# Kernel optimization log

Hardware: AMD Instinct MI355X
Metric: run time of the kernel (lower is better)

Reference implementation:

```python
import jax, jax.numpy as jnp
import numpy as np

N_NODES = 100000
NEG_SLOPE = 0.01  # F.leaky_relu default


def _gin_mean_layer(x, src, dst):
    """DGL GINConv(aggregator='mean', apply_func=None, eps=0, activation=leaky_relu).
    out = leaky_relu((1+eps)*x + mean_{in-neighbors} x_src), nodes with no in-edges get mean=0.
    """
    msg_sum = jax.ops.segment_sum(x[src], dst, num_segments=N_NODES)  # [N, D]
    deg = jax.ops.segment_sum(jnp.ones(src.shape, dtype=x.dtype), dst, num_segments=N_NODES)  # [N]
    mean = msg_sum / jnp.maximum(deg, 1.0)[:, None]
    return jax.nn.leaky_relu(x + mean, negative_slope=NEG_SLOPE)


def setup_inputs() -> dict:
    key = jax.random.key(0)
    k0, k1, k2, k3, k4 = jax.random.split(key, 5)
    n_edges = 640000
    d = 128
    return {
        "node_features": jax.random.normal(k0, (N_NODES, d), dtype=jnp.float32),
        "edges1_src": jax.random.randint(k1, (n_edges,), 0, N_NODES, dtype=jnp.int64),
        "edges1_dst": jax.random.randint(k2, (n_edges,), 0, N_NODES, dtype=jnp.int64),
        "edges2_src": jax.random.randint(k3, (n_edges,), 0, N_NODES, dtype=jnp.int64),
        "edges2_dst": jax.random.randint(k4, (n_edges,), 0, N_NODES, dtype=jnp.int64),
    }


def reference(node_features, edges1_src, edges1_dst, edges2_src, edges2_dst):
    h_AC1 = _gin_mean_layer(node_features, edges1_src, edges1_dst)
    h_CA1 = _gin_mean_layer(node_features, edges2_src, edges2_dst)
    h = jnp.concatenate((h_AC1, h_CA1), axis=1)  # [N, 2D]
    h_AC2 = _gin_mean_layer(h, edges1_src, edges1_dst)
    h_CA2 = _gin_mean_layer(h, edges2_src, edges2_dst)
    return jnp.concatenate((h_AC2, h_CA2), axis=1)  # [N, 4D]
```

## Files before the change

kernel.cpp:

```cpp
#include <hip/hip_runtime.h>

#define N_NODES 100000
#define NEG 0.01f
#define CAP 32

typedef float f4v __attribute__((ext_vector_type(4)));

__device__ __forceinline__ float lrelu(float v) { return v > 0.f ? v : NEG * v; }

__device__ __forceinline__ unsigned int f2bf(float f) {
    unsigned int x = __float_as_uint(f);
    return (x + 0x7fffu + ((x >> 16) & 1u)) >> 16;
}
__device__ __forceinline__ unsigned int pack2bf(float lo, float hi) {
    return f2bf(lo) | (f2bf(hi) << 16);
}
__device__ __forceinline__ float bf_lo(unsigned int u) { return __uint_as_float(u << 16); }
__device__ __forceinline__ float bf_hi(unsigned int u) { return __uint_as_float(u & 0xffff0000u); }

__device__ __forceinline__ void unpack8(uint4 u, float* f) {
    f[0] = bf_lo(u.x); f[1] = bf_hi(u.x);
    f[2] = bf_lo(u.y); f[3] = bf_hi(u.y);
    f[4] = bf_lo(u.z); f[5] = bf_hi(u.z);
    f[6] = bf_lo(u.w); f[7] = bf_hi(u.w);
}

__global__ void __launch_bounds__(256) build_and_convert(
        const int* __restrict__ s1, const int* __restrict__ d1a, int E1,
        const int* __restrict__ s2, const int* __restrict__ d2a, int E2,
        int* __restrict__ deg1, int* __restrict__ slots1,
        int* __restrict__ deg2, int* __restrict__ slots2,
        const float4* __restrict__ x, uint4* __restrict__ xb, int convBlocks) {
    int b = blockIdx.x;
    if (b < convBlocks) {
        int i = b * 256 + threadIdx.x;
        if (i >= N_NODES * 16) return;
        float4 v0 = x[2 * i];
        float4 v1 = x[2 * i + 1];
        uint4 p;
        p.x = pack2bf(v0.x, v0.y);
        p.y = pack2bf(v0.z, v0.w);
        p.z = pack2bf(v1.x, v1.y);
        p.w = pack2bf(v1.z, v1.w);
        xb[i] = p;
    } else {
        int i = (b - convBlocks) * 256 + threadIdx.x;
        if (i < E1) {
            int d = d1a[i];
            int pos = atomicAdd(&deg1[d], 1);
            if (pos < CAP) slots1[d * CAP + pos] = s1[i];
        }
        int k = i - E1;
        if (k >= 0 && k < E2) {
            int d = d2a[k];
            int pos = atomicAdd(&deg2[d], 1);
            if (pos < CAP) slots2[d * CAP + pos] = s2[k];
        }
    }
}

__global__ void __launch_bounds__(256) layer1(
        const uint4* __restrict__ x4,
        const int* __restrict__ deg1, const int* __restrict__ slots1,
        const int* __restrict__ deg2, const int* __restrict__ slots2,
        uint4* __restrict__ h4) {
    int gid = blockIdx.x * blockDim.x + threadIdx.x;
    int n = gid >> 6;
    if (n >= N_NODES) return;
    int lane = gid & 63;
    int t = lane & 15;
    int g = lane >> 4;

    uint4 xv = x4[(size_t)n * 16 + t];

    int d1 = deg1[n], d2 = deg2[n];
    int m1 = min(d1, CAP), m2 = min(d2, CAP);
    int M = m1 + m2;

    int idx = 0;
    if (lane < m1) idx = slots1[n * CAP + lane];
    else if (lane - m1 < m2) idx = slots2[n * CAP + (lane - m1)];

    float a[8] = {0.f, 0.f, 0.f, 0.f, 0.f, 0.f, 0.f, 0.f};
    float b[8] = {0.f, 0.f, 0.f, 0.f, 0.f, 0.f, 0.f, 0.f};

    int s0 = __shfl(idx, g);
    uint4 u = make_uint4(0u, 0u, 0u, 0u);
    if (g < M) u = x4[(size_t)s0 * 16 + t];
    for (int j0 = 0; j0 < M; j0 += 4) {
        uint4 cur = u;
        int jc = j0 + g;
        bool isA = jc < m1;
        int jn = jc + 4;
        int sn = __shfl(idx, jn & 63);
        u = make_uint4(0u, 0u, 0u, 0u);
        if (jn < M) u = x4[(size_t)sn * 16 + t];
        float f[8]; unpack8(cur, f);
        #pragma unroll
        for (int i = 0; i < 8; ++i) {
            a[i] += isA ? f[i] : 0.f;
            b[i] += isA ? 0.f : f[i];
        }
    }

    #pragma unroll
    for (int i = 0; i < 8; ++i) {
        a[i] += __shfl_xor(a[i], 16);
        a[i] += __shfl_xor(a[i], 32);
        b[i] += __shfl_xor(b[i], 16);
        b[i] += __shfl_xor(b[i], 32);
    }

    float xf[8]; unpack8(xv, xf);
    float r1 = 1.f / (float)max(d1, 1);
    float r2 = 1.f / (float)max(d2, 1);

    if (g == 0) {
        uint4 o;
        o.x = pack2bf(lrelu(xf[0] + a[0] * r1), lrelu(xf[1] + a[1] * r1));
        o.y = pack2bf(lrelu(xf[2] + a[2] * r1), lrelu(xf[3] + a[3] * r1));
        o.z = pack2bf(lrelu(xf[4] + a[4] * r1), lrelu(xf[5] + a[5] * r1));
        o.w = pack2bf(lrelu(xf[6] + a[6] * r1), lrelu(xf[7] + a[7] * r1));
        h4[(size_t)n * 32 + t] = o;
    } else if (g == 1) {
        uint4 o;
        o.x = pack2bf(lrelu(xf[0] + b[0] * r2), lrelu(xf[1] + b[1] * r2));
        o.y = pack2bf(lrelu(xf[2] + b[2] * r2), lrelu(xf[3] + b[3] * r2));
        o.z = pack2bf(lrelu(xf[4] + b[4] * r2), lrelu(xf[5] + b[5] * r2));
        o.w = pack2bf(lrelu(xf[6] + b[6] * r2), lrelu(xf[7] + b[7] * r2));
        h4[(size_t)n * 32 + 16 + t] = o;
    }
}

__global__ void __launch_bounds__(256) layer2(
        const uint4* __restrict__ h4,
        const int* __restrict__ deg1, const int* __restrict__ slots1,
        const int* __restrict__ deg2, const int* __restrict__ slots2,
        float4* __restrict__ out4) {
    int gid = blockIdx.x * blockDim.x + threadIdx.x;
    int n = gid >> 6;
    if (n >= N_NODES) return;
    int lane = gid & 63;
    int t = lane & 31;
    int g = lane >> 5;

    uint4 hv = h4[(size_t)n * 32 + t];

    int d1 = deg1[n], d2 = deg2[n];
    int m1 = min(d1, CAP), m2 = min(d2, CAP);
    int M = m1 + m2;

    int idx = 0;
    if (lane < m1) idx = slots1[n * CAP + lane];
    else if (lane - m1 < m2) idx = slots2[n * CAP + (lane - m1)];

    float a[8] = {0.f, 0.f, 0.f, 0.f, 0.f, 0.f, 0.f, 0.f};
    float b[8] = {0.f, 0.f, 0.f, 0.f, 0.f, 0.f, 0.f, 0.f};

    int s0 = __shfl(idx, g);
    uint4 u = make_uint4(0u, 0u, 0u, 0u);
    if (g < M) u = h4[(size_t)s0 * 32 + t];
    for (int j0 = 0; j0 < M; j0 += 2) {
        uint4 cur = u;
        int jc = j0 + g;
        bool isA = jc < m1;
        int jn = jc + 2;
        int sn = __shfl(idx, jn & 63);
        u = make_uint4(0u, 0u, 0u, 0u);
        if (jn < M) u = h4[(size_t)sn * 32 + t];
        float f[8]; unpack8(cur, f);
        #pragma unroll
        for (int i = 0; i < 8; ++i) {
            a[i] += isA ? f[i] : 0.f;
            b[i] += isA ? 0.f : f[i];
        }
    }

    #pragma unroll
    for (int i = 0; i < 8; ++i) {
        a[i] += __shfl_xor(a[i], 32);
        b[i] += __shfl_xor(b[i], 32);
    }

    float hf[8]; unpack8(hv, hf);
    float r1 = 1.f / (float)max(d1, 1);
    float r2 = 1.f / (float)max(d2, 1);

    f4v* ob = (f4v*)out4;
    if (g == 0) {
        f4v A0 = {lrelu(hf[0] + a[0] * r1), lrelu(hf[1] + a[1] * r1),
                  lrelu(hf[2] + a[2] * r1), lrelu(hf[3] + a[3] * r1)};
        f4v A1 = {lrelu(hf[4] + a[4] * r1), lrelu(hf[5] + a[5] * r1),
                  lrelu(hf[6] + a[6] * r1), lrelu(hf[7] + a[7] * r1)};
        __builtin_nontemporal_store(A0, &ob[(size_t)n * 128 + 2 * t]);
        __builtin_nontemporal_store(A1, &ob[(size_t)n * 128 + 2 * t + 1]);
    } else {
        f4v B0 = {lrelu(hf[0] + b[0] * r2), lrelu(hf[1] + b[1] * r2),
                  lrelu(hf[2] + b[2] * r2), lrelu(hf[3] + b[3] * r2)};
        f4v B1 = {lrelu(hf[4] + b[4] * r2), lrelu(hf[5] + b[5] * r2),
                  lrelu(hf[6] + b[6] * r2), lrelu(hf[7] + b[7] * r2)};
        __builtin_nontemporal_store(B0, &ob[(size_t)n * 128 + 64 + 2 * t]);
        __builtin_nontemporal_store(B1, &ob[(size_t)n * 128 + 64 + 2 * t + 1]);
    }
}

extern "C" void kernel_launch(void* const* d_in, const int* in_sizes, int n_in,
                              void* d_out, int out_size, void* d_ws, size_t ws_size,
                              hipStream_t stream) {
    const float* x = (const float*)d_in[0];
    const int* e1s = (const int*)d_in[1];
    const int* e1d = (const int*)d_in[2];
    const int* e2s = (const int*)d_in[3];
    const int* e2d = (const int*)d_in[4];
    const int E1 = in_sizes[1];
    const int E2 = in_sizes[3];
    float* out = (float*)d_out;

    int* deg1   = (int*)d_ws;
    int* deg2   = deg1 + N_NODES;
    int* slots1 = deg2 + N_NODES;
    int* slots2 = slots1 + (size_t)N_NODES * CAP;
    unsigned int* xb = (unsigned int*)(slots2 + (size_t)N_NODES * CAP);
    unsigned int* hb = xb + (size_t)N_NODES * 64;

    hipMemsetAsync(deg1, 0, 2ull * N_NODES * sizeof(int), stream);

    int convBlocks = (N_NODES * 16 + 255) / 256;
    int edgeBlocks = (E1 + E2 + 255) / 256;
    build_and_convert<<<convBlocks + edgeBlocks, 256, 0, stream>>>(
        e1s, e1d, E1, e2s, e2d, E2, deg1, slots1, deg2, slots2,
        (const float4*)x, (uint4*)xb, convBlocks);

    int blocks = (N_NODES + 3) / 4;
    layer1<<<blocks, 256, 0, stream>>>(
        (const uint4*)xb, deg1, slots1, deg2, slots2, (uint4*)hb);
    layer2<<<blocks, 256, 0, stream>>>(
        (const uint4*)hb, deg1, slots1, deg2, slots2, (float4*)out);
}
```

Before: 521.7 us.

## Batch edge inserts per thread, deepen gather prefetch, load slot lists unconditionally

The edge-building phase now processes several edges per thread with an unrolled loop, and its blocks are scheduled before the bf16 conversion blocks so the atomic-heavy work starts first. Both layer kernels load the two slot lists unconditionally and merge them with a shuffle, which removes the dependent branchy loads. The neighbor-gather loop now keeps two loads in flight instead of one, to hide more of the random-gather latency. The costs are higher register pressure and reads of unused slot entries.

```diff
diff --git a/kernel.cpp b/kernel.cpp
--- a/kernel.cpp
+++ b/kernel.cpp
@@ -3,6 +3,7 @@
 #define N_NODES 100000
 #define NEG 0.01f
 #define CAP 32
+#define EDGE_ILP 8
 
 typedef float f4v __attribute__((ext_vector_type(4)));
 
@@ -30,10 +31,28 @@
         const int* __restrict__ s2, const int* __restrict__ d2a, int E2,
         int* __restrict__ deg1, int* __restrict__ slots1,
         int* __restrict__ deg2, int* __restrict__ slots2,
-        const float4* __restrict__ x, uint4* __restrict__ xb, int convBlocks) {
+        const float4* __restrict__ x, uint4* __restrict__ xb,
+        int edgeBlocks, int edgeThreads) {
     int b = blockIdx.x;
-    if (b < convBlocks) {
-        int i = b * 256 + threadIdx.x;
+    if (b < edgeBlocks) {
+        int tid = b * 256 + threadIdx.x;
+        int E = E1 + E2;
+        #pragma unroll
+        for (int k = 0; k < EDGE_ILP; ++k) {
+            int e = tid + k * edgeThreads;
+            if (e < E1) {
+                int d = d1a[e];
+                int pos = atomicAdd(&deg1[d], 1);
+                if (pos < CAP) slots1[d * CAP + pos] = s1[e];
+            } else if (e < E) {
+                int q = e - E1;
+                int d = d2a[q];
+                int pos = atomicAdd(&deg2[d], 1);
+                if (pos < CAP) slots2[d * CAP + pos] = s2[q];
+            }
+        }
+    } else {
+        int i = (b - edgeBlocks) * 256 + threadIdx.x;
         if (i >= N_NODES * 16) return;
         float4 v0 = x[2 * i];
         float4 v1 = x[2 * i + 1];
@@ -43,19 +62,6 @@
         p.z = pack2bf(v1.x, v1.y);
         p.w = pack2bf(v1.z, v1.w);
         xb[i] = p;
-    } else {
-        int i = (b - convBlocks) * 256 + threadIdx.x;
-        if (i < E1) {
-            int d = d1a[i];
-            int pos = atomicAdd(&deg1[d], 1);
-            if (pos < CAP) slots1[d * CAP + pos] = s1[i];
-        }
-        int k = i - E1;
-        if (k >= 0 && k < E2) {
-            int d = d2a[k];
-            int pos = atomicAdd(&deg2[d], 1);
-            if (pos < CAP) slots2[d * CAP + pos] = s2[k];
-        }
     }
 }
 
@@ -70,31 +76,36 @@
     int lane = gid & 63;
     int t = lane & 15;
     int g = lane >> 4;
-
+    int lane31 = lane & 31;
+
+    int d1 = deg1[n], d2 = deg2[n];
+    int v1 = slots1[n * CAP + lane31];
+    int v2 = slots2[n * CAP + lane31];
     uint4 xv = x4[(size_t)n * 16 + t];
 
-    int d1 = deg1[n], d2 = deg2[n];
     int m1 = min(d1, CAP), m2 = min(d2, CAP);
     int M = m1 + m2;
 
-    int idx = 0;
-    if (lane < m1) idx = slots1[n * CAP + lane];
-    else if (lane - m1 < m2) idx = slots2[n * CAP + (lane - m1)];
+    int from2 = __shfl(v2, (lane - m1) & 63);
+    int idx = (lane < m1) ? v1 : from2;
 
     float a[8] = {0.f, 0.f, 0.f, 0.f, 0.f, 0.f, 0.f, 0.f};
     float b[8] = {0.f, 0.f, 0.f, 0.f, 0.f, 0.f, 0.f, 0.f};
 
-    int s0 = __shfl(idx, g);
-    uint4 u = make_uint4(0u, 0u, 0u, 0u);
-    if (g < M) u = x4[(size_t)s0 * 16 + t];
+    int sA = __shfl(idx, g);
+    int sB = __shfl(idx, (g + 4) & 63);
+    uint4 u0 = make_uint4(0u, 0u, 0u, 0u);
+    uint4 u1 = make_uint4(0u, 0u, 0u, 0u);
+    if (g < M)     u0 = x4[(size_t)sA * 16 + t];
+    if (g + 4 < M) u1 = x4[(size_t)sB * 16 + t];
     for (int j0 = 0; j0 < M; j0 += 4) {
-        uint4 cur = u;
+        uint4 cur = u0; u0 = u1;
         int jc = j0 + g;
         bool isA = jc < m1;
-        int jn = jc + 4;
+        int jn = jc + 8;
         int sn = __shfl(idx, jn & 63);
-        u = make_uint4(0u, 0u, 0u, 0u);
-        if (jn < M) u = x4[(size_t)sn * 16 + t];
+        u1 = make_uint4(0u, 0u, 0u, 0u);
+        if (jn < M) u1 = x4[(size_t)sn * 16 + t];
         float f[8]; unpack8(cur, f);
         #pragma unroll
         for (int i = 0; i < 8; ++i) {
@@ -143,31 +154,36 @@
     int lane = gid & 63;
     int t = lane & 31;
     int g = lane >> 5;
-
+    int lane31 = lane & 31;
+
+    int d1 = deg1[n], d2 = deg2[n];
+    int v1 = slots1[n * CAP + lane31];
+    int v2 = slots2[n * CAP + lane31];
     uint4 hv = h4[(size_t)n * 32 + t];
 
-    int d1 = deg1[n], d2 = deg2[n];
     int m1 = min(d1, CAP), m2 = min(d2, CAP);
     int M = m1 + m2;
 
-    int idx = 0;
-    if (lane < m1) idx = slots1[n * CAP + lane];
-    else if (lane - m1 < m2) idx = slots2[n * CAP + (lane - m1)];
+    int from2 = __shfl(v2, (lane - m1) & 63);
+    int idx = (lane < m1) ? v1 : from2;
 
     float a[8] = {0.f, 0.f, 0.f, 0.f, 0.f, 0.f, 0.f, 0.f};
     float b[8] = {0.f, 0.f, 0.f, 0.f, 0.f, 0.f, 0.f, 0.f};
 
-    int s0 = __shfl(idx, g);
-    uint4 u = make_uint4(0u, 0u, 0u, 0u);
-    if (g < M) u = h4[(size_t)s0 * 32 + t];
+    int sA = __shfl(idx, g);
+    int sB = __shfl(idx, (g + 2) & 63);
+    uint4 u0 = make_uint4(0u, 0u, 0u, 0u);
+    uint4 u1 = make_uint4(0u, 0u, 0u, 0u);
+    if (g < M)     u0 = h4[(size_t)sA * 32 + t];
+    if (g + 2 < M) u1 = h4[(size_t)sB * 32 + t];
     for (int j0 = 0; j0 < M; j0 += 2) {
-        uint4 cur = u;
+        uint4 cur = u0; u0 = u1;
         int jc = j0 + g;
         bool isA = jc < m1;
-        int jn = jc + 2;
+        int jn = jc + 4;
         int sn = __shfl(idx, jn & 63);
-        u = make_uint4(0u, 0u, 0u, 0u);
-        if (jn < M) u = h4[(size_t)sn * 32 + t];
+        u1 = make_uint4(0u, 0u, 0u, 0u);
+        if (jn < M) u1 = h4[(size_t)sn * 32 + t];
         float f[8]; unpack8(cur, f);
         #pragma unroll
         for (int i = 0; i < 8; ++i) {
@@ -226,10 +242,11 @@
     hipMemsetAsync(deg1, 0, 2ull * N_NODES * sizeof(int), stream);
 
     int convBlocks = (N_NODES * 16 + 255) / 256;
-    int edgeBlocks = (E1 + E2 + 255) / 256;
-    build_and_convert<<<convBlocks + edgeBlocks, 256, 0, stream>>>(
+    int edgeThreads = ((E1 + E2 + EDGE_ILP - 1) / EDGE_ILP + 255) / 256 * 256;
+    int edgeBlocks = edgeThreads / 256;
+    build_and_convert<<<edgeBlocks + convBlocks, 256, 0, stream>>>(
         e1s, e1d, E1, e2s, e2d, E2, deg1, slots1, deg2, slots2,
-        (const float4*)x, (uint4*)xb, convBlocks);
+        (const float4*)x, (uint4*)xb, edgeBlocks, edgeThreads);
 
     int blocks = (N_NODES + 3) / 4;
     layer1<<<blocks, 256, 0, stream>>>(
```

Measured after the change: 486.3 us. -6.8%, faster.
